# Optimization experiments

Measured on AMD Instinct MI355X. Metric: run time of the kernel, lower is better.

The kernel has to match this reference:

```python
import jax, jax.numpy as jnp
import numpy as np

DIM = 256
NUM_HEADS = 8
HEAD_DIM = DIM // NUM_HEADS


def setup_inputs() -> dict:
    key = jax.random.key(0)
    k_x, k_wq, k_bq, k_wp, k_bp = jax.random.split(key, 5)
    x = jax.random.normal(k_x, (4, DIM, 64, 64), dtype=jnp.float32)
    # 1x1 convs == per-pixel linear layers over channels
    w_qkv = jax.random.normal(k_wq, (3 * DIM, DIM), dtype=jnp.float32) * (DIM ** -0.5)
    b_qkv = jax.random.normal(k_bq, (3 * DIM,), dtype=jnp.float32) * 0.02
    w_proj = jax.random.normal(k_wp, (DIM, DIM), dtype=jnp.float32) * (DIM ** -0.5)
    b_proj = jax.random.normal(k_bp, (DIM,), dtype=jnp.float32) * 0.02
    return {"x": x, "w_qkv": w_qkv, "b_qkv": b_qkv, "w_proj": w_proj, "b_proj": b_proj}


def reference(x, w_qkv, b_qkv, w_proj, b_proj):
    B, C, H, W = x.shape
    S = H * W
    h, d = NUM_HEADS, HEAD_DIM
    # flatten spatial dims: (B, C, H, W) -> (B, S, C)
    xf = x.reshape(B, C, S).transpose(0, 2, 1)
    # 1x1 conv qkv: (B, S, 3C)
    qkv = xf @ w_qkv.T + b_qkv
    q, k, v = jnp.split(qkv, 3, axis=-1)
    # channel dim splits as (heads, head_dim): (B, S, C) -> (B, h, S, d)
    split = lambda t: t.reshape(B, S, h, d).transpose(0, 2, 1, 3)
    q, k, v = split(q), split(k), split(v)
    scale = d ** -0.5
    attn = jnp.einsum('bhsd,bhtd->bhst', q, k) * scale  # (B, h, S, S)
    attn = jax.nn.softmax(attn, axis=-1)
    out = jnp.einsum('bhst,bhtd->bhsd', attn, v)
    # merge heads: (B, h, S, d) -> (B, S, C)
    out = out.transpose(0, 2, 1, 3).reshape(B, S, C)
    out = out @ w_proj.T + b_proj
    # back to (B, C, H, W)
    return out.transpose(0, 2, 1).reshape(B, C, H, W)
```

## Files before the change

kernel.cpp:

```cpp
#include <hip/hip_runtime.h>


typedef __attribute__((ext_vector_type(8))) short short8;
typedef __attribute__((ext_vector_type(4))) float f4;

__device__ __forceinline__ short f2bs(float f) {
  union { float f; unsigned u; } v; v.f = f;
  unsigned r = v.u + 0x7FFFu + ((v.u >> 16) & 1u);
  return (short)(r >> 16);
}

__device__ __forceinline__ short8 cvt8(f4 a, f4 b) {
  short8 o;
  o[0] = f2bs(a[0]); o[1] = f2bs(a[1]); o[2] = f2bs(a[2]); o[3] = f2bs(a[3]);
  o[4] = f2bs(b[0]); o[5] = f2bs(b[1]); o[6] = f2bs(b[2]); o[7] = f2bs(b[3]);
  return o;
}

__global__ __launch_bounds__(256) void k_qkv(
    const float* __restrict__ x, const float* __restrict__ w,
    const float* __restrict__ bias,
    short* __restrict__ Qr, short* __restrict__ Kq, short* __restrict__ Vt) {
  const int tid = threadIdx.x;
  const int L = tid & 63, wv = tid >> 6;
  const int ln15 = L & 15, quad = L >> 4;
  const int mt = blockIdx.x;
  const int b = mt >> 6;
  const int s0 = (mt & 63) << 6;
  const int j0 = blockIdx.y << 6;
  const int jw = j0 + wv * 16;

  __shared__ __align__(16) short tl[4 * 64 * 16];

  f4 acc[4] = {{0,0,0,0},{0,0,0,0},{0,0,0,0},{0,0,0,0}};
  const float* wb = w + (jw + ln15) * 256 + quad * 8;
  const float* xb = x + b * (256 * 4096) + s0 + ln15;

#pragma unroll 2
  for (int cb = 0; cb < 256; cb += 32) {
    f4 a0 = *(const f4*)(wb + cb);
    f4 a1 = *(const f4*)(wb + cb + 4);
    short8 af = cvt8(a0, a1);
    const float* xc = xb + (cb + quad * 8) * 4096;
#pragma unroll
    for (int sub = 0; sub < 4; ++sub) {
      const float* xs = xc + sub * 16;
      short8 bf;
#pragma unroll
      for (int jj = 0; jj < 8; ++jj) bf[jj] = f2bs(xs[jj * 4096]);
      acc[sub] = __builtin_amdgcn_mfma_f32_16x16x32_bf16(af, bf, acc[sub], 0, 0, 0);
    }
  }

  float bj[4];
#pragma unroll
  for (int r = 0; r < 4; ++r) bj[r] = bias[jw + quad * 4 + r];

  const int type = j0 >> 8;
  if (type == 2) {
    const int jv = jw - 512;
    const int h = jv >> 5;
    const int dbase = jv & 31;
#pragma unroll
    for (int r = 0; r < 4; ++r) {
      const int d = dbase + quad * 4 + r;
      short* vp = Vt + (size_t)((b * 8 + h) * 32 + d) * 4096 + s0 + ln15;
#pragma unroll
      for (int sub = 0; sub < 4; ++sub)
        vp[sub * 16] = f2bs(acc[sub][r] + bj[r]);
    }
  } else {
    const float qsc = 0.17677669529663689f * 1.44269504088896f;
    const float mul = (type == 0) ? qsc : 1.0f;
    short* dst = (type == 0) ? Qr : Kq;
    const int hj = jw & 255;
    short* tw = tl + wv * 1024;
#pragma unroll
    for (int sub = 0; sub < 4; ++sub) {
      const int s = sub * 16 + ln15;
      const int swz = (s >> 2) & 1;
#pragma unroll
      for (int r = 0; r < 4; ++r) {
        const int dl = quad * 4 + r;
        tw[s * 16 + (((dl >> 3) ^ swz) * 8) + (dl & 7)] = f2bs((acc[sub][r] + bj[r]) * mul);
      }
    }
    const int h = hj >> 5;
    const int d0 = hj & 31;
#pragma unroll
    for (int i = 0; i < 2; ++i) {
      const int sl = i * 32 + (L >> 1);
      const int gg = L & 1;
      const int g2 = gg ^ ((sl >> 2) & 1);
      short8 row = *(const short8*)(tw + sl * 16 + g2 * 8);
      *(short8*)(dst + (size_t)((b * 8 + h) * 4096 + s0 + sl) * 32 + d0 + gg * 8) = row;
    }
  }
}

__global__ __launch_bounds__(256, 5) void k_attn(
    const short* __restrict__ Qr, const short* __restrict__ Kq,
    const short* __restrict__ Vt, short* __restrict__ O) {
  const int tid = threadIdx.x;
  const int L = tid & 63, wv = tid >> 6;
  const int ln15 = L & 15, quad = L >> 4;
  const int p = blockIdx.y * 64 + blockIdx.x;
  const int bh = (p & 7) * 4 + (p >> 9);
  const int qblk = (p >> 3) & 63;
  const int b = bh >> 3, h = bh & 7;
  const int qt = wv & 1, half = wv >> 1;
  const int qb = qblk * 64 + qt * 32;

  const short* Qb = Qr + (size_t)bh * 4096 * 32;
  const short* Kb = Kq + (size_t)bh * 4096 * 32 + half * 2048 * 32;
  const short* Vb = Vt + (size_t)bh * 32 * 4096 + half * 2048;

  __shared__ float cbuf[2][32 * 33];
  __shared__ float l_up[2][32];

  short8 qf[2];
#pragma unroll
  for (int qs = 0; qs < 2; ++qs)
    qf[qs] = *(const short8*)(Qb + (qb + qs * 16 + ln15) * 32 + quad * 8);

  short8 ones;
#pragma unroll
  for (int j = 0; j < 8; ++j) ones[j] = (short)0x3F80;

  f4 acc[2][2] = {{{0,0,0,0},{0,0,0,0}},{{0,0,0,0},{0,0,0,0}}};
  f4 accl[2] = {{0,0,0,0},{0,0,0,0}};
  const f4 z4 = {0.f, 0.f, 0.f, 0.f};

  const short* kp = Kb + ln15 * 32 + quad * 8;
  const short* vp = Vb + ln15 * 4096 + quad * 8;

  auto loadK = [&](int kb, short8* kr) {
#pragma unroll
    for (int t = 0; t < 4; ++t)
      kr[t] = *(const short8*)(kp + (kb + t * 16) * 32);
  };

  auto chunk = [&](int kb, const short8* kr) {
    short8 vf[4];
#pragma unroll
    for (int f = 0; f < 2; ++f)
#pragma unroll
      for (int dg = 0; dg < 2; ++dg)
        vf[f * 2 + dg] = *(const short8*)(vp + dg * (16 * 4096) + kb + f * 32);

#pragma unroll
    for (int qs = 0; qs < 2; ++qs) {
      int dwa[4][2];
#pragma unroll
      for (int t = 0; t < 4; ++t) {
        f4 sc = __builtin_amdgcn_mfma_f32_16x16x32_bf16(kr[t], qf[qs], z4, 0, 0, 0);
        float p0 = __builtin_amdgcn_exp2f(sc[0]);
        float p1 = __builtin_amdgcn_exp2f(sc[1]);
        float p2 = __builtin_amdgcn_exp2f(sc[2]);
        float p3 = __builtin_amdgcn_exp2f(sc[3]);
        asm("v_cvt_pk_bf16_f32 %0, %1, %2" : "=v"(dwa[t][0]) : "v"(p0), "v"(p1));
        asm("v_cvt_pk_bf16_f32 %0, %1, %2" : "=v"(dwa[t][1]) : "v"(p2), "v"(p3));
      }
      union { int i[4]; short8 s; } pk[2];
#pragma unroll
      for (int f = 0; f < 2; ++f)
#pragma unroll
        for (int u = 0; u < 2; ++u) {
          int a = dwa[2 * f][u];
          int c = dwa[2 * f + 1][u];
          asm("v_permlane32_swap_b32 %0, %1" : "+v"(a), "+v"(c));
          asm("v_permlane16_swap_b32 %0, %1" : "+v"(a), "+v"(c));
          pk[f].i[u] = a;
          pk[f].i[u + 2] = c;
        }
      accl[qs] = __builtin_amdgcn_mfma_f32_16x16x32_bf16(pk[0].s, ones, accl[qs], 0, 0, 0);
      accl[qs] = __builtin_amdgcn_mfma_f32_16x16x32_bf16(pk[1].s, ones, accl[qs], 0, 0, 0);
      acc[qs][0] = __builtin_amdgcn_mfma_f32_16x16x32_bf16(pk[0].s, vf[0], acc[qs][0], 0, 0, 0);
      acc[qs][1] = __builtin_amdgcn_mfma_f32_16x16x32_bf16(pk[0].s, vf[1], acc[qs][1], 0, 0, 0);
      acc[qs][0] = __builtin_amdgcn_mfma_f32_16x16x32_bf16(pk[1].s, vf[2], acc[qs][0], 0, 0, 0);
      acc[qs][1] = __builtin_amdgcn_mfma_f32_16x16x32_bf16(pk[1].s, vf[3], acc[qs][1], 0, 0, 0);
    }
  };

  short8 kf0[4], kf1[4];
  loadK(0, kf0);
#pragma unroll 1
  for (int kb = 0; kb < 1920; kb += 128) {
    loadK(kb + 64, kf1);
    chunk(kb, kf0);
    loadK(kb + 128, kf0);
    chunk(kb + 64, kf1);
  }
  loadK(1984, kf1);
  chunk(1920, kf0);
  chunk(1984, kf1);

  if (half == 1) {
    float* cw = cbuf[qt];
#pragma unroll
    for (int qs = 0; qs < 2; ++qs) {
#pragma unroll
      for (int dg = 0; dg < 2; ++dg)
#pragma unroll
        for (int r = 0; r < 4; ++r)
          cw[(qs * 16 + quad * 4 + r) * 33 + dg * 16 + ln15] = acc[qs][dg][r];
      if (ln15 == 0) {
#pragma unroll
        for (int r = 0; r < 4; ++r)
          l_up[qt][qs * 16 + quad * 4 + r] = accl[qs][r];
      }
    }
  }
  __syncthreads();
  if (half == 0) {
    const float* cu = cbuf[qt];
#pragma unroll
    for (int qs = 0; qs < 2; ++qs) {
#pragma unroll
      for (int r = 0; r < 4; ++r) {
        const float lup = l_up[qt][qs * 16 + quad * 4 + r];
        const float rl = 1.0f / (accl[qs][r] + lup);
        const int sg = qb + qs * 16 + quad * 4 + r;
        short* op = O + (size_t)(b * 4096 + sg) * 256 + h * 32 + ln15;
        const int ci = (qs * 16 + quad * 4 + r) * 33 + ln15;
        op[0]  = f2bs((acc[qs][0][r] + cu[ci]) * rl);
        op[16] = f2bs((acc[qs][1][r] + cu[ci + 16]) * rl);
      }
    }
  }
}

__global__ __launch_bounds__(256) void k_proj(
    const short* __restrict__ O, const float* __restrict__ w,
    const float* __restrict__ bias, float* __restrict__ out) {
  const int tid = threadIdx.x;
  const int L = tid & 63, wv = tid >> 6;
  const int ln15 = L & 15, quad = L >> 4;
  const int m0 = blockIdx.x * 64 + wv * 16;
  const int n0 = blockIdx.y << 6;
  const int b = m0 >> 12, s0 = m0 & 4095;

  f4 acc[4] = {{0,0,0,0},{0,0,0,0},{0,0,0,0},{0,0,0,0}};
  const short* Ob = O + (size_t)(m0 + ln15) * 256 + quad * 8;
  const float* wb = w + (n0 + ln15) * 256 + quad * 8;

#pragma unroll 2
  for (int cb = 0; cb < 256; cb += 32) {
    short8 af = *(const short8*)(Ob + cb);
#pragma unroll
    for (int sub = 0; sub < 4; ++sub) {
      f4 b0 = *(const f4*)(wb + sub * (16 * 256) + cb);
      f4 b1 = *(const f4*)(wb + sub * (16 * 256) + cb + 4);
      short8 bf = cvt8(b0, b1);
      acc[sub] = __builtin_amdgcn_mfma_f32_16x16x32_bf16(af, bf, acc[sub], 0, 0, 0);
    }
  }

  __shared__ float tl[4][64 * 17];
  float* tw = tl[wv];
#pragma unroll
  for (int sub = 0; sub < 4; ++sub) {
    const float bv = bias[n0 + sub * 16 + ln15];
#pragma unroll
    for (int r = 0; r < 4; ++r)
      tw[(sub * 16 + ln15) * 17 + quad * 4 + r] = acc[sub][r] + bv;
  }
#pragma unroll
  for (int i = 0; i < 4; ++i) {
    const int c = i * 16 + (L >> 2);
    const int ms = (L & 3) * 4;
    f4 v;
#pragma unroll
    for (int j = 0; j < 4; ++j) v[j] = tw[c * 17 + ms + j];
    *(f4*)(out + (size_t)b * (256 * 4096) + (size_t)(n0 + c) * 4096 + s0 + ms) = v;
  }
}

extern "C" void kernel_launch(void* const* d_in, const int* in_sizes, int n_in,
                              void* d_out, int out_size, void* d_ws, size_t ws_size,
                              hipStream_t stream) {
  const float* x      = (const float*)d_in[0];
  const float* w_qkv  = (const float*)d_in[1];
  const float* b_qkv  = (const float*)d_in[2];
  const float* w_proj = (const float*)d_in[3];
  const float* b_proj = (const float*)d_in[4];
  float* out = (float*)d_out;

  const size_t SEG = (size_t)4 * 8 * 4096 * 32;
  short* Qr = (short*)d_ws;
  short* Kq = Qr + SEG;
  short* Vt = Kq + SEG;
  short* O  = Vt + SEG;

  k_qkv <<<dim3(256, 12), 256, 0, stream>>>(x, w_qkv, b_qkv, Qr, Kq, Vt);
  k_attn<<<dim3(64, 32),  256, 0, stream>>>(Qr, Kq, Vt, O);
  k_proj<<<dim3(256, 4),  256, 0, stream>>>(O, w_proj, b_proj, out);
}
```

Baseline: 332.6 us.

## Restructure attention inner loop to prefetch K and V one chunk ahead

Replaces the lambda-based double-buffered K loop with an explicit 128-key loop. It computes QK^T and exp for both query sub-tiles before issuing the next K loads, and prefetches V fragments one 64-key chunk ahead of their PV MFMAs. It also relaxes launch bounds from 5 to 4 waves-per-EU minimum, freeing registers for the extra live prefetch buffers at the cost of occupancy. The last iteration issues prefetch loads past the head's key range. Those values are unused, but for the final batch-head they may read beyond the end of the buffer.

Measured after the change: 329.7 us. No clear change (-0.9%).

```diff
diff --git a/kernel.cpp b/kernel.cpp
--- a/kernel.cpp
+++ b/kernel.cpp
@@ -98,7 +98,7 @@
   }
 }
 
-__global__ __launch_bounds__(256, 5) void k_attn(
+__global__ __launch_bounds__(256, 4) void k_attn(
     const short* __restrict__ Qr, const short* __restrict__ Kq,
     const short* __restrict__ Vt, short* __restrict__ O) {
   const int tid = threadIdx.x;
@@ -112,7 +112,7 @@
   const int qb = qblk * 64 + qt * 32;
 
   const short* Qb = Qr + (size_t)bh * 4096 * 32;
-  const short* Kb = Kq + (size_t)bh * 4096 * 32 + half * 2048 * 32;
+  const short* Kb = Kq + (size_t)bh * 4096 * 32 + half * (2048 * 32);
   const short* Vb = Vt + (size_t)bh * 32 * 4096 + half * 2048;
 
   __shared__ float cbuf[2][32 * 33];
@@ -134,40 +134,44 @@
   const short* kp = Kb + ln15 * 32 + quad * 8;
   const short* vp = Vb + ln15 * 4096 + quad * 8;
 
-  auto loadK = [&](int kb, short8* kr) {
-#pragma unroll
-    for (int t = 0; t < 4; ++t)
-      kr[t] = *(const short8*)(kp + (kb + t * 16) * 32);
-  };
-
-  auto chunk = [&](int kb, const short8* kr) {
-    short8 vf[4];
-#pragma unroll
-    for (int f = 0; f < 2; ++f)
-#pragma unroll
-      for (int dg = 0; dg < 2; ++dg)
-        vf[f * 2 + dg] = *(const short8*)(vp + dg * (16 * 4096) + kb + f * 32);
-
-#pragma unroll
-    for (int qs = 0; qs < 2; ++qs) {
-      int dwa[4][2];
+  short8 kfA[4], kfB[4], vf[4];
+#pragma unroll
+  for (int t = 0; t < 4; ++t) kfA[t] = *(const short8*)(kp + (t * 16) * 32);
+#pragma unroll
+  for (int f = 0; f < 2; ++f) {
+    vf[f * 2]     = *(const short8*)(vp + f * 32);
+    vf[f * 2 + 1] = *(const short8*)(vp + 16 * 4096 + f * 32);
+  }
+#pragma unroll
+  for (int t = 0; t < 4; ++t) kfB[t] = *(const short8*)(kp + (64 + t * 16) * 32);
+
+#pragma unroll 1
+  for (int kb = 0; kb < 2048; kb += 128) {
+    int dwa[2][4][2];
+#pragma unroll
+    for (int qs = 0; qs < 2; ++qs)
 #pragma unroll
       for (int t = 0; t < 4; ++t) {
-        f4 sc = __builtin_amdgcn_mfma_f32_16x16x32_bf16(kr[t], qf[qs], z4, 0, 0, 0);
+        f4 sc = __builtin_amdgcn_mfma_f32_16x16x32_bf16(kfA[t], qf[qs], z4, 0, 0, 0);
         float p0 = __builtin_amdgcn_exp2f(sc[0]);
         float p1 = __builtin_amdgcn_exp2f(sc[1]);
         float p2 = __builtin_amdgcn_exp2f(sc[2]);
         float p3 = __builtin_amdgcn_exp2f(sc[3]);
-        asm("v_cvt_pk_bf16_f32 %0, %1, %2" : "=v"(dwa[t][0]) : "v"(p0), "v"(p1));
-        asm("v_cvt_pk_bf16_f32 %0, %1, %2" : "=v"(dwa[t][1]) : "v"(p2), "v"(p3));
-      }
+        asm("v_cvt_pk_bf16_f32 %0, %1, %2" : "=v"(dwa[qs][t][0]) : "v"(p0), "v"(p1));
+        asm("v_cvt_pk_bf16_f32 %0, %1, %2" : "=v"(dwa[qs][t][1]) : "v"(p2), "v"(p3));
+      }
+#pragma unroll
+    for (int t = 0; t < 4; ++t)
+      kfA[t] = *(const short8*)(kp + (kb + 128 + t * 16) * 32);
+#pragma unroll
+    for (int qs = 0; qs < 2; ++qs) {
       union { int i[4]; short8 s; } pk[2];
 #pragma unroll
       for (int f = 0; f < 2; ++f)
 #pragma unroll
         for (int u = 0; u < 2; ++u) {
-          int a = dwa[2 * f][u];
-          int c = dwa[2 * f + 1][u];
+          int a = dwa[qs][2 * f][u];
+          int c = dwa[qs][2 * f + 1][u];
           asm("v_permlane32_swap_b32 %0, %1" : "+v"(a), "+v"(c));
           asm("v_permlane16_swap_b32 %0, %1" : "+v"(a), "+v"(c));
           pk[f].i[u] = a;
@@ -180,20 +184,54 @@
       acc[qs][0] = __builtin_amdgcn_mfma_f32_16x16x32_bf16(pk[1].s, vf[2], acc[qs][0], 0, 0, 0);
       acc[qs][1] = __builtin_amdgcn_mfma_f32_16x16x32_bf16(pk[1].s, vf[3], acc[qs][1], 0, 0, 0);
     }
-  };
-
-  short8 kf0[4], kf1[4];
-  loadK(0, kf0);
-#pragma unroll 1
-  for (int kb = 0; kb < 1920; kb += 128) {
-    loadK(kb + 64, kf1);
-    chunk(kb, kf0);
-    loadK(kb + 128, kf0);
-    chunk(kb + 64, kf1);
-  }
-  loadK(1984, kf1);
-  chunk(1920, kf0);
-  chunk(1984, kf1);
+#pragma unroll
+    for (int f = 0; f < 2; ++f) {
+      vf[f * 2]     = *(const short8*)(vp + kb + 64 + f * 32);
+      vf[f * 2 + 1] = *(const short8*)(vp + 16 * 4096 + kb + 64 + f * 32);
+    }
+
+#pragma unroll
+    for (int qs = 0; qs < 2; ++qs)
+#pragma unroll
+      for (int t = 0; t < 4; ++t) {
+        f4 sc = __builtin_amdgcn_mfma_f32_16x16x32_bf16(kfB[t], qf[qs], z4, 0, 0, 0);
+        float p0 = __builtin_amdgcn_exp2f(sc[0]);
+        float p1 = __builtin_amdgcn_exp2f(sc[1]);
+        float p2 = __builtin_amdgcn_exp2f(sc[2]);
+        float p3 = __builtin_amdgcn_exp2f(sc[3]);
+        asm("v_cvt_pk_bf16_f32 %0, %1, %2" : "=v"(dwa[qs][t][0]) : "v"(p0), "v"(p1));
+        asm("v_cvt_pk_bf16_f32 %0, %1, %2" : "=v"(dwa[qs][t][1]) : "v"(p2), "v"(p3));
+      }
+#pragma unroll
+    for (int t = 0; t < 4; ++t)
+      kfB[t] = *(const short8*)(kp + (kb + 192 + t * 16) * 32);
+#pragma unroll
+    for (int qs = 0; qs < 2; ++qs) {
+      union { int i[4]; short8 s; } pk[2];
+#pragma unroll
+      for (int f = 0; f < 2; ++f)
+#pragma unroll
+        for (int u = 0; u < 2; ++u) {
+          int a = dwa[qs][2 * f][u];
+          int c = dwa[qs][2 * f + 1][u];
+          asm("v_permlane32_swap_b32 %0, %1" : "+v"(a), "+v"(c));
+          asm("v_permlane16_swap_b32 %0, %1" : "+v"(a), "+v"(c));
+          pk[f].i[u] = a;
+          pk[f].i[u + 2] = c;
+        }
+      accl[qs] = __builtin_amdgcn_mfma_f32_16x16x32_bf16(pk[0].s, ones, accl[qs], 0, 0, 0);
+      accl[qs] = __builtin_amdgcn_mfma_f32_16x16x32_bf16(pk[1].s, ones, accl[qs], 0, 0, 0);
+      acc[qs][0] = __builtin_amdgcn_mfma_f32_16x16x32_bf16(pk[0].s, vf[0], acc[qs][0], 0, 0, 0);
+      acc[qs][1] = __builtin_amdgcn_mfma_f32_16x16x32_bf16(pk[0].s, vf[1], acc[qs][1], 0, 0, 0);
+      acc[qs][0] = __builtin_amdgcn_mfma_f32_16x16x32_bf16(pk[1].s, vf[2], acc[qs][0], 0, 0, 0);
+      acc[qs][1] = __builtin_amdgcn_mfma_f32_16x16x32_bf16(pk[1].s, vf[3], acc[qs][1], 0, 0, 0);
+    }
+#pragma unroll
+    for (int f = 0; f < 2; ++f) {
+      vf[f * 2]     = *(const short8*)(vp + kb + 128 + f * 32);
+      vf[f * 2 + 1] = *(const short8*)(vp + 16 * 4096 + kb + 128 + f * 32);
+    }
+  }
 
   if (half == 1) {
     float* cw = cbuf[qt];
```
